# Kernel optimization log

Hardware: AMD Instinct MI355X
Metric: run time of the kernel (lower is better)

Reference implementation:

```python
import jax, jax.numpy as jnp
import numpy as np

DIM = 512
HEADS = 8
DIM_HEAD = 64
H_DIM = HEADS * DIM_HEAD  # 512
SCALE = DIM_HEAD ** -0.5


def setup_inputs() -> dict:
    key = jax.random.key(0)
    k_x, k_qkv, k_out, k_b = jax.random.split(key, 4)
    N, C, L = 4, DIM, 2048
    x = jax.random.normal(k_x, (N, C, L), dtype=jnp.float32)
    # Conv1d kernel_size=1 weights, kernel dim squeezed: [out_ch, in_ch]
    w_qkv = jax.random.normal(k_qkv, (3 * H_DIM, DIM), dtype=jnp.float32) * (DIM ** -0.5)
    w_out = jax.random.normal(k_out, (DIM, H_DIM), dtype=jnp.float32) * (H_DIM ** -0.5)
    b_out = jax.random.normal(k_b, (DIM,), dtype=jnp.float32) * 0.01
    return {"x": x, "w_qkv": w_qkv, "w_out": w_out, "b_out": b_out}


def reference(x, w_qkv, w_out, b_out):
    N, C, L = x.shape
    # 1x1 conv == pointwise linear over channels
    qkv = jnp.einsum('oc,ncl->nol', w_qkv, x)            # N, 3*h_dim, L
    q, k, v = jnp.split(qkv, 3, axis=1)                  # each N, h_dim, L
    # split heads: N, h, d, L
    q = q.reshape(N, HEADS, DIM_HEAD, L) * SCALE
    k = k.reshape(N, HEADS, DIM_HEAD, L)
    v = v.reshape(N, HEADS, DIM_HEAD, L)
    sim = jnp.einsum('nhdi,nhdj->nhij', q, k)            # N, h, L, L
    attn = jax.nn.softmax(sim, axis=-1)                  # stable softmax (max-subtract fused)
    out = jnp.einsum('nhij,nhdj->nhid', attn, v)         # N, h, L, d
    # 'b h l c -> b (h c) l'
    out = jnp.transpose(out, (0, 1, 3, 2)).reshape(N, H_DIM, L)
    return jnp.einsum('oc,ncl->nol', w_out, out) + b_out[None, :, None]
```

## Files before the change

### kernel.cpp

```cpp
#include <hip/hip_runtime.h>
#include <hip/hip_bf16.h>
#include <stdint.h>
#include <stddef.h>

typedef unsigned short u16;
typedef __bf16 bf16x8 __attribute__((ext_vector_type(8)));
typedef __bf16 bf16x2 __attribute__((ext_vector_type(2)));
typedef float f32x4 __attribute__((ext_vector_type(4)));
typedef unsigned short u16x8 __attribute__((ext_vector_type(8)));
typedef unsigned short u16x4 __attribute__((ext_vector_type(4)));

#define NBATCH 4
#define LSEQ   2048
#define CDIM   512
#define NHEADS 8
#define DHEAD  64
#define QSCALE 0.18033688011112042f

__device__ __forceinline__ float exp2_hw(float x) {
  return __builtin_amdgcn_exp2f(x);
}

__device__ __forceinline__ u16 f2bf(float f) {
  union { float f; unsigned u; } v; v.f = f;
  return (u16)((v.u + 0x7FFFu + ((v.u >> 16) & 1u)) >> 16);
}
__device__ __forceinline__ u16 f2bf_hw(float f) {
  union { __bf16 b; u16 u; } cv; cv.b = (__bf16)f; return cv.u;
}
__device__ __forceinline__ unsigned pack2bf(float a, float b) {
  union { bf16x2 v; unsigned u; } cv;
  cv.v[0] = (__bf16)a; cv.v[1] = (__bf16)b;
  return cv.u;
}
__device__ __forceinline__ f32x4 mfma16(bf16x8 a, bf16x8 b, f32x4 c) {
  return __builtin_amdgcn_mfma_f32_16x16x32_bf16(a, b, c, 0, 0, 0);
}
__device__ __forceinline__ void async16(const u16* gp, const u16* lp) {
  auto* g = reinterpret_cast<const __attribute__((address_space(1))) uint32_t*>(
      reinterpret_cast<uintptr_t>(gp));
  auto* l = reinterpret_cast<__attribute__((address_space(3))) uint32_t*>(
      reinterpret_cast<uintptr_t>(lp));
  __builtin_amdgcn_global_load_lds(g, l, 16, 0, 0);
}

__global__ __launch_bounds__(256) void prep(const float* __restrict__ x,
                                            const float* __restrict__ wqkv,
                                            const float* __restrict__ wout,
                                            u16* __restrict__ xT,
                                            u16* __restrict__ wqkvb,
                                            u16* __restrict__ woutb) {
  __shared__ u16 tile[32][36];
  int b = blockIdx.x, t = threadIdx.x;
  if (b < 4096) {
    int lb = b & 63, cb = (b >> 6) & 15, n = b >> 10;
    int c = t >> 3, lq = (t & 7) * 4;
    float4 f = *(const float4*)(x + ((size_t)(n * CDIM + cb * 32 + c)) * LSEQ + lb * 32 + lq);
    u16x4 cv;
    cv[0] = f2bf(f.x); cv[1] = f2bf(f.y); cv[2] = f2bf(f.z); cv[3] = f2bf(f.w);
    *(u16x4*)&tile[c][lq] = cv;
    __syncthreads();
    int l = t >> 3, cq = (t & 7) * 4;
    u16x4 o;
    o[0] = tile[cq + 0][l]; o[1] = tile[cq + 1][l];
    o[2] = tile[cq + 2][l]; o[3] = tile[cq + 3][l];
    *(u16x4*)(xT + ((size_t)(n * LSEQ + lb * 32 + l)) * CDIM + cb * 32 + cq) = o;
  } else {
    int i = (b - 4096) * 256 + t;
    const float4* src;
    u16* dst;
    int idx;
    if (i < 196608) { src = (const float4*)wqkv; dst = wqkvb; idx = i; }
    else            { src = (const float4*)wout; dst = woutb; idx = i - 196608; }
    float4 f = src[idx];
    u16x4 o;
    o[0] = f2bf(f.x); o[1] = f2bf(f.y); o[2] = f2bf(f.z); o[3] = f2bf(f.w);
    *(u16x4*)(dst + (size_t)idx * 4) = o;
  }
}

__global__ __launch_bounds__(256, 3) void qkv_gemm(const u16* __restrict__ wqkvb,
                                                   const u16* __restrict__ xT,
                                                   u16* __restrict__ qT,
                                                   u16* __restrict__ kT,
                                                   u16* __restrict__ vp) {
  __shared__ __align__(16) u16 lds[17408];
  u16* At = lds;
  u16* Bt = lds + 8192;

  int mb = blockIdx.y, lb = blockIdx.x, n = blockIdx.z;
  int o0 = mb * 128, l0 = lb * 128;
  int t = threadIdx.x, w = t >> 6, lane = t & 63, quad = lane >> 4, l15 = lane & 15;
  int wr = w >> 1, wc = w & 1;
  int lr = lane >> 3, lc = lane & 7;
  int swzS = (lc ^ lr) * 8;
  int swzR = l15 & 7;

  const u16* ag = wqkvb + (size_t)(o0 + w * 32 + lr) * CDIM + swzS;
  const u16* bg = xT + ((size_t)n * LSEQ + l0 + w * 32 + lr) * CDIM + swzS;

  f32x4 acc[4][4];
#pragma unroll
  for (int i = 0; i < 4; ++i)
#pragma unroll
    for (int j = 0; j < 4; ++j) acc[i][j] = (f32x4)0.0f;

  for (int k0 = 0; k0 < CDIM; k0 += 64) {
#pragma unroll
    for (int g = 0; g < 4; ++g) {
      async16(ag + (size_t)g * 8 * CDIM + k0, At + (w * 32 + g * 8) * 64);
      async16(bg + (size_t)g * 8 * CDIM + k0, Bt + (w * 32 + g * 8) * 64);
    }
    __syncthreads();
    bf16x8 af[4][2], bf[4][2];
#pragma unroll
    for (int rt = 0; rt < 4; ++rt)
#pragma unroll
      for (int kk = 0; kk < 2; ++kk) {
        af[rt][kk] = *(const bf16x8*)&At[(wr * 64 + rt * 16 + l15) * 64 +
                                         (((kk * 4 + quad) ^ swzR) * 8)];
        bf[rt][kk] = *(const bf16x8*)&Bt[(wc * 64 + rt * 16 + l15) * 64 +
                                         (((kk * 4 + quad) ^ swzR) * 8)];
      }
#pragma unroll
    for (int kk = 0; kk < 2; ++kk)
#pragma unroll
      for (int rt = 0; rt < 4; ++rt)
#pragma unroll
        for (int ct = 0; ct < 4; ++ct)
          acc[rt][ct] = mfma16(af[rt][kk], bf[ct][kk], acc[rt][ct]);
    __syncthreads();
  }

  int seg = mb >> 2;
  int hb = (mb & 3) * 2;
  if (seg < 2) {
    float scale = (seg == 0) ? QSCALE : 1.0f;
#pragma unroll
    for (int rt = 0; rt < 4; ++rt)
#pragma unroll
      for (int ct = 0; ct < 4; ++ct) {
        u16x4 ov;
#pragma unroll
        for (int r = 0; r < 4; ++r) ov[r] = f2bf_hw(acc[rt][ct][r] * scale);
        *(u16x4*)&lds[(wc * 64 + ct * 16 + l15) * 136 + wr * 64 + rt * 16 + quad * 4] = ov;
      }
    __syncthreads();
    u16* dst0 = (seg == 0) ? qT : kT;
#pragma unroll
    for (int p = 0; p < 8; ++p) {
      int l = p * 16 + (t >> 4);
      int ch = t & 15;
      u16x8 val = *(const u16x8*)&lds[l * 136 + ch * 8];
      int h = hb + (ch >> 3);
      int d = (ch & 7) * 8;
      *(u16x8*)(dst0 + (((size_t)(n * NHEADS + h)) * LSEQ + l0 + l) * DHEAD + d) = val;
    }
  } else {
#pragma unroll
    for (int rt = 0; rt < 4; ++rt)
#pragma unroll
      for (int ct = 0; ct < 4; ++ct)
#pragma unroll
        for (int r = 0; r < 4; ++r)
          lds[(wr * 64 + rt * 16 + quad * 4 + r) * 136 + wc * 64 + ct * 16 + l15] =
              f2bf_hw(acc[rt][ct][r]);
    __syncthreads();
#pragma unroll
    for (int p = 0; p < 8; ++p) {
      int o = p * 16 + (t >> 4);
      int ch = t & 15;
      u16x8 val = *(const u16x8*)&lds[o * 136 + ch * 8];
      int h = hb + (o >> 6);
      int d = o & 63;
      *(u16x8*)(vp + (((size_t)(n * NHEADS + h)) * DHEAD + d) * LSEQ + l0 + ch * 8) = val;
    }
  }
}

__global__ __launch_bounds__(256, 2) void attn_kernel(const u16* __restrict__ qT,
                                                      const u16* __restrict__ kT,
                                                      const u16* __restrict__ vp,
                                                      u16* __restrict__ aoT) {
  __shared__ __align__(16) u16 KVs[3][8192];

  int h = blockIdx.x, ib = blockIdx.y, n = blockIdx.z;
  int i0 = ib * 128;
  const u16* qb = qT + ((size_t)(n * NHEADS + h)) * LSEQ * DHEAD;
  const u16* kb = kT + ((size_t)(n * NHEADS + h)) * LSEQ * DHEAD;
  const u16* vb = vp + ((size_t)(n * NHEADS + h)) * DHEAD * LSEQ;
  int t = threadIdx.x, w = t >> 6, lane = t & 63, quad = lane >> 4, l15 = lane & 15;
  int wi = w >> 1, wj = w & 1;

  bf16x8 qf[4][2];
#pragma unroll
  for (int it = 0; it < 4; ++it)
#pragma unroll
    for (int kk = 0; kk < 2; ++kk)
      qf[it][kk] = *(const bf16x8*)(qb + (size_t)(i0 + wi * 64 + it * 16 + l15) * DHEAD +
                                    kk * 32 + quad * 8);

  f32x4 Oc[4][4];
#pragma unroll
  for (int it = 0; it < 4; ++it)
#pragma unroll
    for (int dt = 0; dt < 4; ++dt) Oc[it][dt] = (f32x4)0.0f;
  float lsum[4] = {0.f, 0.f, 0.f, 0.f};

  int lr = lane >> 3, lc = lane & 7;
  int swz = lc ^ lr;
  const u16* kgl = kb + lr * DHEAD + swz * 8;
  const u16* vgl = vb + (size_t)lr * LSEQ + swz * 8;
  int swzK = l15 & 7;

  auto stage = [&](int j0, int b) {
#pragma unroll
    for (int s = 0; s < 2; ++s) {
      int g = s * 4 + w;
      async16(kgl + (size_t)j0 * DHEAD + g * 512, &KVs[b][g * 512]);
      async16(vgl + j0 + (size_t)g * 8 * LSEQ, &KVs[b][4096 + g * 512]);
    }
  };

  bf16x8 pf_c[4];
  bf16x8 vf_c[4];

  auto tile_body = [&](int tt, bool do_pv) {
    const u16* Kt = &KVs[tt % 3][0];
    const u16* Vt = &KVs[tt % 3][4096];

    bf16x8 kf[2][2];
#pragma unroll
    for (int jt = 0; jt < 2; ++jt)
#pragma unroll
      for (int kk = 0; kk < 2; ++kk)
        kf[jt][kk] = *(const bf16x8*)&Kt[(wj * 32 + 16 * jt + l15) * 64 +
                                         (((quad + 4 * kk) ^ swzK) * 8)];

    if (do_pv) {
#pragma unroll
      for (int it = 0; it < 4; ++it)
#pragma unroll
        for (int dt = 0; dt < 4; ++dt)
          Oc[it][dt] = mfma16(vf_c[dt], pf_c[it], Oc[it][dt]);
    }

    f32x4 st[4][2];
#pragma unroll
    for (int it = 0; it < 4; ++it)
#pragma unroll
      for (int jt = 0; jt < 2; ++jt) {
        f32x4 s = (f32x4)0.0f;
        s = mfma16(kf[jt][0], qf[it][0], s);
        s = mfma16(kf[jt][1], qf[it][1], s);
        st[it][jt] = s;
      }

#pragma unroll
    for (int dt = 0; dt < 4; ++dt)
      vf_c[dt] = *(const bf16x8*)&Vt[(16 * dt + l15) * 64 +
                                     (((wj * 4 + quad) ^ swzK) * 8)];

#pragma unroll
    for (int it = 0; it < 4; ++it) {
      unsigned wjh[2][2];
#pragma unroll
      for (int jt = 0; jt < 2; ++jt) {
        float p0 = exp2_hw(st[it][jt][0]);
        float p1 = exp2_hw(st[it][jt][1]);
        float p2 = exp2_hw(st[it][jt][2]);
        float p3 = exp2_hw(st[it][jt][3]);
        lsum[it] += (p0 + p1) + (p2 + p3);
        wjh[jt][0] = pack2bf(p0, p1);
        wjh[jt][1] = pack2bf(p2, p3);
      }
      unsigned a0 = wjh[0][0], b0 = wjh[1][0];
      unsigned a1 = wjh[0][1], b1 = wjh[1][1];
      asm volatile("v_permlane32_swap_b32 %0, %1" : "+v"(a0), "+v"(b0));
      asm volatile("v_permlane16_swap_b32 %0, %1" : "+v"(a0), "+v"(b0));
      asm volatile("v_permlane32_swap_b32 %0, %1" : "+v"(a1), "+v"(b1));
      asm volatile("v_permlane16_swap_b32 %0, %1" : "+v"(a1), "+v"(b1));
      union { unsigned u[4]; bf16x8 v; } cv;
      cv.u[0] = a0; cv.u[1] = a1; cv.u[2] = b0; cv.u[3] = b1;
      pf_c[it] = cv.v;
    }
  };

  stage(0, 0);
  stage(64, 1);

  asm volatile("s_waitcnt vmcnt(4)" ::: "memory");
  __builtin_amdgcn_s_barrier();
  __builtin_amdgcn_sched_barrier(0);
  stage(128, 2);
  tile_body(0, false);

  for (int tt = 1; tt < 31; ++tt) {
    asm volatile("s_waitcnt vmcnt(4)" ::: "memory");
    __builtin_amdgcn_s_barrier();
    __builtin_amdgcn_sched_barrier(0);
    if (tt + 2 < 32) stage((tt + 2) * 64, (tt + 2) % 3);
    tile_body(tt, true);
  }

  asm volatile("s_waitcnt vmcnt(0)" ::: "memory");
  __builtin_amdgcn_s_barrier();
  __builtin_amdgcn_sched_barrier(0);
  tile_body(31, true);

#pragma unroll
  for (int it = 0; it < 4; ++it)
#pragma unroll
    for (int dt = 0; dt < 4; ++dt)
      Oc[it][dt] = mfma16(vf_c[dt], pf_c[it], Oc[it][dt]);

#pragma unroll
  for (int it = 0; it < 4; ++it) {
    lsum[it] += __shfl_xor(lsum[it], 16, 64);
    lsum[it] += __shfl_xor(lsum[it], 32, 64);
  }
  __syncthreads();
  float* Os = (float*)&KVs[0][0];
  float* Ls = (float*)((char*)&KVs[0][0] + 40960);
  if (wj == 1) {
#pragma unroll
    for (int it = 0; it < 4; ++it) {
#pragma unroll
      for (int dt = 0; dt < 4; ++dt)
        *(f32x4*)&Os[((((wi * 4 + it) * 4 + dt) * 16) + l15) * 20 + 4 * quad] =
            Oc[it][dt];
      if (quad == 0) Ls[(wi * 4 + it) * 16 + l15] = lsum[it];
    }
  }
  __syncthreads();
  if (wj == 0) {
#pragma unroll
    for (int it = 0; it < 4; ++it) {
      float lt = lsum[it] + Ls[(wi * 4 + it) * 16 + l15];
      float inv = 1.0f / lt;
      int row = i0 + wi * 64 + it * 16 + l15;
#pragma unroll
      for (int dt = 0; dt < 4; ++dt) {
        f32x4 part = *(const f32x4*)&Os[((((wi * 4 + it) * 4 + dt) * 16) + l15) * 20 +
                                        4 * quad];
        u16x4 ov;
#pragma unroll
        for (int r = 0; r < 4; ++r)
          ov[r] = f2bf_hw((Oc[it][dt][r] + part[r]) * inv);
        *(u16x4*)(aoT + ((size_t)n * LSEQ + row) * CDIM + h * DHEAD + 16 * dt +
                  4 * quad) = ov;
      }
    }
  }
}

__global__ __launch_bounds__(256) void out_gemm(const u16* __restrict__ woutb,
                                                const u16* __restrict__ aoT,
                                                const float* __restrict__ bout,
                                                float* __restrict__ out) {
  __shared__ __align__(16) u16 lds[49152];

  int mb = blockIdx.y, lb = blockIdx.x, n = blockIdx.z;
  int o0 = mb * 128, l0 = lb * 128;
  int t = threadIdx.x, w = t >> 6, lane = t & 63, quad = lane >> 4, l15 = lane & 15;
  int wr = w >> 1, wc = w & 1;
  int lr = lane >> 3, lc = lane & 7;
  int swzS = (lc ^ lr) * 8;
  int swzR = l15 & 7;

  const u16* ag = woutb + (size_t)(o0 + w * 32 + lr) * CDIM + swzS;
  const u16* bg = aoT + ((size_t)n * LSEQ + l0 + w * 32 + lr) * CDIM + swzS;

  f32x4 acc[4][4];
#pragma unroll
  for (int i = 0; i < 4; ++i)
#pragma unroll
    for (int j = 0; j < 4; ++j) acc[i][j] = (f32x4)0.0f;

  auto stage = [&](int ks, int b) {
    u16* At = lds + b * 16384;
    u16* Bt = At + 8192;
#pragma unroll
    for (int g = 0; g < 4; ++g) {
      async16(ag + (size_t)g * 8 * CDIM + ks * 64, At + (w * 32 + g * 8) * 64);
      async16(bg + (size_t)g * 8 * CDIM + ks * 64, Bt + (w * 32 + g * 8) * 64);
    }
  };

  auto body = [&](int ks) {
    const u16* At = lds + (ks % 3) * 16384;
    const u16* Bt = At + 8192;
    bf16x8 af[4][2], bf[4][2];
#pragma unroll
    for (int rt = 0; rt < 4; ++rt)
#pragma unroll
      for (int kk = 0; kk < 2; ++kk) {
        af[rt][kk] = *(const bf16x8*)&At[(wr * 64 + rt * 16 + l15) * 64 +
                                         (((kk * 4 + quad) ^ swzR) * 8)];
        bf[rt][kk] = *(const bf16x8*)&Bt[(wc * 64 + rt * 16 + l15) * 64 +
                                         (((kk * 4 + quad) ^ swzR) * 8)];
      }
#pragma unroll
    for (int kk = 0; kk < 2; ++kk)
#pragma unroll
      for (int rt = 0; rt < 4; ++rt)
#pragma unroll
        for (int ct = 0; ct < 4; ++ct)
          acc[rt][ct] = mfma16(af[rt][kk], bf[ct][kk], acc[rt][ct]);
  };

  stage(0, 0);
  stage(1, 1);

  asm volatile("s_waitcnt vmcnt(8)" ::: "memory");
  __builtin_amdgcn_s_barrier();
  __builtin_amdgcn_sched_barrier(0);
  stage(2, 2);
  body(0);

  for (int ks = 1; ks < 7; ++ks) {
    asm volatile("s_waitcnt vmcnt(8)" ::: "memory");
    __builtin_amdgcn_s_barrier();
    __builtin_amdgcn_sched_barrier(0);
    if (ks + 2 < 8) stage(ks + 2, (ks + 2) % 3);
    body(ks);
  }

  asm volatile("s_waitcnt vmcnt(0)" ::: "memory");
  __builtin_amdgcn_s_barrier();
  __builtin_amdgcn_sched_barrier(0);
  body(7);

#pragma unroll
  for (int rt = 0; rt < 4; ++rt) {
    int orow = o0 + wr * 64 + rt * 16 + quad * 4;
#pragma unroll
    for (int r = 0; r < 4; ++r) {
      float bb = bout[orow + r];
      float* orow_p = out + ((size_t)n * CDIM + orow + r) * LSEQ + l0 + wc * 64;
#pragma unroll
      for (int ct = 0; ct < 4; ++ct)
        orow_p[ct * 16 + l15] = acc[rt][ct][r] + bb;
    }
  }
}

extern "C" void kernel_launch(void* const* d_in, const int* in_sizes, int n_in,
                              void* d_out, int out_size, void* d_ws, size_t ws_size,
                              hipStream_t stream) {
  (void)in_sizes; (void)n_in; (void)out_size; (void)ws_size;
  const float* x    = (const float*)d_in[0];
  const float* wqkv = (const float*)d_in[1];
  const float* wout = (const float*)d_in[2];
  const float* bout = (const float*)d_in[3];

  char* ws = (char*)d_ws;
  u16* xT    = (u16*)(ws + 0);
  u16* wqkvb = (u16*)(ws + 8388608);
  u16* woutb = (u16*)(ws + 9961472);
  u16* qT    = (u16*)(ws + 10485760);
  u16* kT    = (u16*)(ws + 18874368);
  u16* vp    = (u16*)(ws + 27262976);
  u16* aoT   = (u16*)(ws + 35651584);

  hipLaunchKernelGGL(prep, dim3(5120), dim3(256), 0, stream, x, wqkv, wout, xT, wqkvb, woutb);
  hipLaunchKernelGGL(qkv_gemm, dim3(16, 12, 4), dim3(256), 0, stream, wqkvb, xT, qT, kT, vp);
  hipLaunchKernelGGL(attn_kernel, dim3(8, 16, 4), dim3(256), 0, stream, qT, kT, vp, aoT);
  hipLaunchKernelGGL(out_gemm, dim3(16, 4, 4), dim3(256), 0, stream, woutb, aoT, bout,
                     (float*)d_out);
}
```

Measured before the change: 140.7 us.

## Double-buffer QKV GEMM LDS tiles with async prefetch two stages ahead

Splits the QKV projection GEMM's shared memory into two buffers, so the async global-to-LDS loads for the next k-slice are issued while MFMAs run on the current slice. Explicit vmcnt waits and barriers replace the per-iteration syncthreads pair. This hides load latency at the cost of twice the LDS per block, and launch bounds drop from 3 to 2 blocks per CU. The QKV GEMM is only part of the total pipeline, which also includes the attention and output projection.

```diff
diff --git a/kernel.cpp b/kernel.cpp
--- a/kernel.cpp
+++ b/kernel.cpp
@@ -79,14 +79,12 @@
   }
 }
 
-__global__ __launch_bounds__(256, 3) void qkv_gemm(const u16* __restrict__ wqkvb,
+__global__ __launch_bounds__(256, 2) void qkv_gemm(const u16* __restrict__ wqkvb,
                                                    const u16* __restrict__ xT,
                                                    u16* __restrict__ qT,
                                                    u16* __restrict__ kT,
                                                    u16* __restrict__ vp) {
-  __shared__ __align__(16) u16 lds[17408];
-  u16* At = lds;
-  u16* Bt = lds + 8192;
+  __shared__ __align__(16) u16 lds[32768];
 
   int mb = blockIdx.y, lb = blockIdx.x, n = blockIdx.z;
   int o0 = mb * 128, l0 = lb * 128;
@@ -105,13 +103,19 @@
 #pragma unroll
     for (int j = 0; j < 4; ++j) acc[i][j] = (f32x4)0.0f;
 
-  for (int k0 = 0; k0 < CDIM; k0 += 64) {
+  auto stage = [&](int ks, int b) {
+    u16* At = lds + b * 16384;
+    u16* Bt = At + 8192;
 #pragma unroll
     for (int g = 0; g < 4; ++g) {
-      async16(ag + (size_t)g * 8 * CDIM + k0, At + (w * 32 + g * 8) * 64);
-      async16(bg + (size_t)g * 8 * CDIM + k0, Bt + (w * 32 + g * 8) * 64);
-    }
-    __syncthreads();
+      async16(ag + (size_t)g * 8 * CDIM + ks * 64, At + (w * 32 + g * 8) * 64);
+      async16(bg + (size_t)g * 8 * CDIM + ks * 64, Bt + (w * 32 + g * 8) * 64);
+    }
+  };
+
+  auto body = [&](int ks) {
+    const u16* At = lds + (ks & 1) * 16384;
+    const u16* Bt = At + 8192;
     bf16x8 af[4][2], bf[4][2];
 #pragma unroll
     for (int rt = 0; rt < 4; ++rt)
@@ -129,8 +133,40 @@
 #pragma unroll
         for (int ct = 0; ct < 4; ++ct)
           acc[rt][ct] = mfma16(af[rt][kk], bf[ct][kk], acc[rt][ct]);
-    __syncthreads();
-  }
+  };
+
+  stage(0, 0);
+  stage(1, 1);
+
+  asm volatile("s_waitcnt vmcnt(8)" ::: "memory");
+  __builtin_amdgcn_s_barrier();
+  __builtin_amdgcn_sched_barrier(0);
+  body(0);
+  __builtin_amdgcn_s_barrier();
+  __builtin_amdgcn_sched_barrier(0);
+  stage(2, 0);
+
+  for (int ks = 1; ks < 6; ++ks) {
+    asm volatile("s_waitcnt vmcnt(8)" ::: "memory");
+    __builtin_amdgcn_s_barrier();
+    __builtin_amdgcn_sched_barrier(0);
+    body(ks);
+    __builtin_amdgcn_s_barrier();
+    __builtin_amdgcn_sched_barrier(0);
+    stage(ks + 2, ks & 1);
+  }
+
+  asm volatile("s_waitcnt vmcnt(8)" ::: "memory");
+  __builtin_amdgcn_s_barrier();
+  __builtin_amdgcn_sched_barrier(0);
+  body(6);
+
+  asm volatile("s_waitcnt vmcnt(0)" ::: "memory");
+  __builtin_amdgcn_s_barrier();
+  __builtin_amdgcn_sched_barrier(0);
+  body(7);
+
+  __syncthreads();
 
   int seg = mb >> 2;
   int hb = (mb & 3) * 2;
```

Result: no change. 139.8 us (-0.6%).
